# Kernel tuning notes

Measured on AMD Instinct MI355X. Metric: run time of the kernel, lower is better.

The kernel has to match this reference:

```python
import jax, jax.numpy as jnp
import numpy as np

K = 8            # hard-coded knn k
NS = 0.2         # LeakyReLU negative slope
EPS = 1e-6
LN_EPS = 1e-5
H = 6            # num_heads


def vn_lin(W, x):
    # VNLinear: linear over vector-channel dim (axis 1). x: (B, Cin, 3, ...)
    return jnp.einsum('oc,bc...->bo...', W, x)


def vn_leaky(x, W, U):
    # VNLinearLeakyReLU (no BN): feature map p, direction map d
    p = vn_lin(W, x)
    d = vn_lin(U, x)
    dot = jnp.sum(p * d, axis=2, keepdims=True)
    dsq = jnp.sum(d * d, axis=2, keepdims=True)
    neg = p - (dot / (dsq + EPS)) * d
    return NS * p + (1.0 - NS) * jnp.where(dot >= 0, p, neg)


def vn_layernorm(x, g, b):
    # LayerNorm on per-channel vector norms, rescale directions. x: (B,C,3,N)
    n = jnp.sqrt(jnp.sum(x * x, axis=2) + EPS)            # (B,C,N)
    mu = jnp.mean(n, axis=1, keepdims=True)
    var = jnp.var(n, axis=1, keepdims=True)
    nhat = (n - mu) / jnp.sqrt(var + LN_EPS)
    nnew = g[None, :, None] * nhat + b[None, :, None]
    return x * (nnew / n)[:, :, None, :]


def vn_attention(vn_x, Wq, Wk, Wv, Wo):
    # vn_x: (B, C, 3, N); VNLinear(C, 3C) projections, multi-head SDPA over N
    B, C, _, N = vn_x.shape
    def heads(W):
        t = vn_lin(W, vn_x)                               # (B, 3C, 3, N)
        t = t.reshape(B, H, 3 * C // H, 3, N)
        return t.transpose(0, 1, 4, 2, 3).reshape(B, H, N, -1)  # (B,H,N,9C/H)
    q, k, v = heads(Wq), heads(Wk), heads(Wv)
    scale = (3 * C // H) ** -0.5                          # head_dim = dim//H = 64
    attn = jax.nn.softmax(jnp.einsum('bhqd,bhkd->bhqk', q, k) * scale, axis=-1)
    o = jnp.einsum('bhqk,bhkd->bhqd', attn, v)            # (B,H,N,9C/H)
    o = o.transpose(0, 2, 1, 3).reshape(B, N, 3 * C, 3).transpose(0, 2, 3, 1)
    return vn_lin(Wo, o)                                  # (B, C, 3, N)


def vn_get_graph_feature(x, knn_index):
    # x: (B, C, 3, N); knn_index: flat (B*K*N,) into (B*N) rows
    B, C, _, N = x.shape
    xp = x.transpose(0, 3, 1, 2).reshape(B * N, C * 3)
    feat = xp[knn_index].reshape(B, K, N, C, 3)
    xc = x.transpose(0, 3, 1, 2).reshape(B, 1, N, C, 3)
    f = jnp.concatenate([feat - xc, jnp.broadcast_to(xc, (B, K, N, C, 3))], axis=3)
    return f.transpose(0, 3, 4, 2, 1)                     # (B, 2C, 3, N, K)


def setup_inputs() -> dict:
    key = jax.random.key(0)
    ks = jax.random.split(key, 20)
    B, N, C = 4, 2048, 128
    def w(k, o, i):
        return jax.random.normal(k, (o, i), jnp.float32) * (i ** -0.5)
    return {
        'x': jax.random.normal(ks[0], (B, N, 3 * C), jnp.float32),
        'knn_index': jax.random.randint(ks[1], (B * K * N,), 0, B * N),
        'g1': jnp.ones((C,), jnp.float32), 'b1': jnp.zeros((C,), jnp.float32),
        'g2': jnp.ones((C,), jnp.float32), 'b2': jnp.zeros((C,), jnp.float32),
        'Wq': w(ks[2], 3 * C, C), 'Wk': w(ks[3], 3 * C, C), 'Wv': w(ks[4], 3 * C, C),
        'Wo': w(ks[5], C, 3 * C),
        'W1': w(ks[6], C, 2 * C), 'U1': w(ks[7], C, 2 * C),   # conv1: 256->128
        'W2': w(ks[8], C, 2 * C),                               # conv2: 256->128
        'W3': w(ks[9], 2 * C, C), 'U3': w(ks[10], 2 * C, C),   # conv3: 128->256
        'W4': w(ks[11], C, 2 * C), 'U4': w(ks[12], C, 2 * C),  # conv4: 256->128
    }


def reference(x, knn_index, g1, b1, g2, b2, Wq, Wk, Wv, Wo, W1, U1, W2, W3, U3, W4, U4):
    B, N, D = x.shape
    C = D // 3
    vn_x = x.transpose(0, 2, 1).reshape(B, C, 3, N)
    norm_x = vn_layernorm(vn_x, g1, b1)
    x_1 = vn_attention(norm_x, Wq, Wk, Wv, Wo)            # (B,C,3,N)
    knn_f = vn_get_graph_feature(norm_x, knn_index)       # (B,2C,3,N,K)
    knn_f = vn_leaky(knn_f, W1, U1)                       # (B,C,3,N,K)
    knn_f = jnp.mean(knn_f, axis=-1)                      # mean_pool over k
    x_1 = jnp.concatenate([x_1, knn_f], axis=1)           # (B,2C,3,N)
    x_1 = vn_lin(W2, x_1)                                 # (B,C,3,N)
    vn_x = vn_x + x_1
    nx2 = vn_layernorm(vn_x, g2, b2)
    h = vn_leaky(nx2, W3, U3)                             # (B,2C,3,N)
    h = vn_leaky(h, W4, U4)                               # (B,C,3,N)
    vn_x = vn_x + h
    return vn_x.reshape(B, D, N).transpose(0, 2, 1)       # (B,N,384)
```

## Files before the change

### kernel.cpp

```cpp
#include <hip/hip_runtime.h>
#include <math.h>

#define NFIX 2048
#define HH 6
#define KNN 8
#define NSLOPE 0.2f
#define EPSF 1e-6f
#define LNEPSF 1e-5f
#define QSCALE 0.18033688011112042f

typedef unsigned short ushort_t;
typedef unsigned int uint_t;
typedef __attribute__((ext_vector_type(8))) short bf16x8;
typedef __attribute__((ext_vector_type(4))) short bf16x4;
typedef __attribute__((ext_vector_type(8))) _Float16 f16x8;
typedef __attribute__((ext_vector_type(4))) _Float16 f16x4;
typedef __attribute__((ext_vector_type(16))) float f32x16;
typedef __attribute__((ext_vector_type(4))) float f32x4;

__device__ __forceinline__ ushort_t f2bf(float f) {
  union { float f; unsigned u; } v; v.f = f;
  unsigned r = v.u + 0x7fff + ((v.u >> 16) & 1);
  return (ushort_t)(r >> 16);
}
__device__ __forceinline__ float bf2f(ushort_t u) {
  union { uint_t u; float f; } v; v.u = ((uint_t)u) << 16; return v.f;
}
__device__ __forceinline__ uint_t pack2(float a, float b) {
  return (uint_t)f2bf(a) | ((uint_t)f2bf(b) << 16);
}
__device__ __forceinline__ uint_t packh2(float a, float b) {
  union { _Float16 h; ushort_t s; } ha, hb;
  ha.h = (_Float16)a; hb.h = (_Float16)b;
  return (uint_t)ha.s | ((uint_t)hb.s << 16);
}

__device__ __forceinline__ void vnleaky3(const float* p, const float* dv, float* out) {
  float dot = p[0]*dv[0] + p[1]*dv[1] + p[2]*dv[2];
  float dsq = dv[0]*dv[0] + dv[1]*dv[1] + dv[2]*dv[2] + EPSF;
  float f = dot / dsq;
#pragma unroll
  for (int d = 0; d < 3; ++d) {
    float neg = p[d] - f * dv[d];
    out[d] = NSLOPE * p[d] + (1.f - NSLOPE) * ((dot >= 0.f) ? p[d] : neg);
  }
}

__global__ void prep_weights(const float* __restrict__ Wq, const float* __restrict__ Wk,
                             const float* __restrict__ Wv, const float* __restrict__ Wo,
                             const float* __restrict__ W1, const float* __restrict__ U1,
                             const float* __restrict__ W2, const float* __restrict__ W3,
                             const float* __restrict__ U3, const float* __restrict__ W4,
                             const float* __restrict__ U4,
                             ushort_t* __restrict__ Wall, _Float16* __restrict__ Af16,
                             _Float16* __restrict__ W3h, _Float16* __restrict__ U3h,
                             _Float16* __restrict__ W4h, _Float16* __restrict__ U4h) {
  int idx = blockIdx.x * 256 + threadIdx.x;
  if (idx < 212992) {
    int m = idx >> 7, c = idx & 127;
    float val;
    if (m < 384)       val = Wq[m*128 + c] * QSCALE;
    else if (m < 768)  val = Wk[(m-384)*128 + c];
    else if (m < 1152) val = Wv[(m-768)*128 + c];
    else {
      int j = m - 1152;
      if (j < 128)      val = W1[j*256 + c];
      else if (j < 256) val = U1[(j-128)*256 + c];
      else if (j < 384) { int o = j-256; val = W1[o*256 + 128 + c] - W1[o*256 + c]; }
      else              { int o = j-384; val = U1[o*256 + 128 + c] - U1[o*256 + c]; }
    }
    Wall[idx] = f2bf(val); return;
  }
  idx -= 212992;
  if (idx < 49152) {
    int j = idx / 128, c = idx % 128;
    float s = 0.f;
    for (int cp = 0; cp < 128; ++cp) s += W2[c*256 + cp] * Wo[cp*384 + j];
    Af16[(size_t)c*512 + j] = (_Float16)s; return;
  }
  idx -= 49152;
  if (idx < 16384) {
    int c2 = idx / 128, c = idx % 128;
    Af16[(size_t)c*512 + 384 + c2] = (_Float16)W2[c*256 + 128 + c2]; return;
  }
  idx -= 16384;
  if (idx < 32768) { W3h[idx] = (_Float16)W3[idx]; return; }
  idx -= 32768;
  if (idx < 32768) { U3h[idx] = (_Float16)U3[idx]; return; }
  idx -= 32768;
  if (idx < 32768) { W4h[idx] = (_Float16)W4[idx]; return; }
  idx -= 32768;
  if (idx < 32768) { U4h[idx] = (_Float16)U4[idx]; return; }
}

__global__ __launch_bounds__(128) void ln1_kernel(const float* __restrict__ in,
                                                  ushort_t* __restrict__ xbp,
                                                  float* __restrict__ xdi,
                                                  const float* __restrict__ g,
                                                  const float* __restrict__ b) {
  int bn = blockIdx.x;
  int c = threadIdx.x;
  const float* row = in + (size_t)bn * 384;
  float x0 = row[c*3+0], x1 = row[c*3+1], x2 = row[c*3+2];
  float nv = sqrtf(x0*x0 + x1*x1 + x2*x2 + EPSF);
  float s1 = nv, s2 = nv*nv;
#pragma unroll
  for (int off = 32; off >= 1; off >>= 1) {
    s1 += __shfl_down(s1, off);
    s2 += __shfl_down(s2, off);
  }
  __shared__ float red[4];
  int lane = threadIdx.x & 63, w = threadIdx.x >> 6;
  if (lane == 0) { red[w*2] = s1; red[w*2+1] = s2; }
  __syncthreads();
  float tot1 = red[0] + red[2], tot2 = red[1] + red[3];
  float mu  = tot1 * (1.f/128.f);
  float var = tot2 * (1.f/128.f) - mu*mu;
  float rsig = rsqrtf(var + LNEPSF);
  float nnew = g[c] * ((nv - mu) * rsig) + b[c];
  float sc = nnew / nv;
  size_t rb = (size_t)bn * 384;
  xbp[rb + c]       = f2bf(x0*sc);
  xbp[rb + 128 + c] = f2bf(x1*sc);
  xbp[rb + 256 + c] = f2bf(x2*sc);
  xdi[rb + c]       = x0;
  xdi[rb + 128 + c] = x1;
  xdi[rb + 256 + c] = x2;
}

__global__ __launch_bounds__(128) void ln2_kernel(const float* __restrict__ in,
                                                  _Float16* __restrict__ out,
                                                  const float* __restrict__ g,
                                                  const float* __restrict__ b) {
  int bn = blockIdx.x;
  int c = threadIdx.x;
  size_t base = (size_t)bn * 384;
  float x0 = in[base + c], x1 = in[base + 128 + c], x2 = in[base + 256 + c];
  float nv = sqrtf(x0*x0 + x1*x1 + x2*x2 + EPSF);
  float s1 = nv, s2 = nv*nv;
#pragma unroll
  for (int off = 32; off >= 1; off >>= 1) {
    s1 += __shfl_down(s1, off);
    s2 += __shfl_down(s2, off);
  }
  __shared__ float red[4];
  int lane = threadIdx.x & 63, w = threadIdx.x >> 6;
  if (lane == 0) { red[w*2] = s1; red[w*2+1] = s2; }
  __syncthreads();
  float tot1 = red[0] + red[2], tot2 = red[1] + red[3];
  float mu  = tot1 * (1.f/128.f);
  float var = tot2 * (1.f/128.f) - mu*mu;
  float rsig = rsqrtf(var + LNEPSF);
  float nnew = g[c] * ((nv - mu) * rsig) + b[c];
  float sc = nnew / nv;
  out[base + c]       = (_Float16)(x0*sc);
  out[base + 128 + c] = (_Float16)(x1*sc);
  out[base + 256 + c] = (_Float16)(x2*sc);
}

#define XT_PITCH 132
#define WT_PITCH 132
#define TR_PITCH 36
__global__ __launch_bounds__(256, 2) void qkv_conv1_mfma(
    const ushort_t* __restrict__ xb, const ushort_t* __restrict__ Wall,
    ushort_t* __restrict__ q, ushort_t* __restrict__ k, ushort_t* __restrict__ v,
    _Float16* __restrict__ YZh, _Float16* __restrict__ NBh) {
  __shared__ ushort_t xs[128*XT_PITCH];
  __shared__ ushort_t wt[32*WT_PITCH];
  __shared__ float tr[4][32*TR_PITCH];
  int nb = blockIdx.x % 192;
  int mq = blockIdx.x / 192;
  int n0 = nb * 128;
  int t = threadIdx.x;
  int w = t >> 6, lane = t & 63, ql = lane & 31, hl = lane >> 5;
  for (int idx = t; idx < 2048; idx += 256) {
    int n = idx >> 4, c16 = idx & 15;
    bf16x8 gv = *(const bf16x8*)&xb[(size_t)(n0 + n)*128 + c16*8];
    ushort_t* dst = &xs[n*XT_PITCH + c16*8];
    *(bf16x4*)dst = __builtin_shufflevector(gv, gv, 0, 1, 2, 3);
    *(bf16x4*)(dst+4) = __builtin_shufflevector(gv, gv, 4, 5, 6, 7);
  }
  __syncthreads();
  bf16x8 xf[8];
  {
    const ushort_t* xr = &xs[(w*32 + ql)*XT_PITCH + hl*8];
#pragma unroll
    for (int cs = 0; cs < 8; ++cs) {
      bf16x4 lo = *(const bf16x4*)(xr + cs*16);
      bf16x4 hi = *(const bf16x4*)(xr + cs*16 + 4);
      xf[cs] = __builtin_shufflevector(lo, hi, 0, 1, 2, 3, 4, 5, 6, 7);
    }
  }
  int ng = n0 + w*32 + ql;
  int pt = ng / 3;
  int d  = ng - 3*pt;
  float* trw = tr[w];
  for (int mt = 0; mt < 13; ++mt) {
    int m0 = mq*416 + mt*32;
    __syncthreads();
    for (int idx = t; idx < 512; idx += 256) {
      int mm = idx >> 4, c16 = idx & 15;
      bf16x8 gv = *(const bf16x8*)&Wall[(size_t)(m0 + mm)*128 + c16*8];
      ushort_t* dst = &wt[mm*WT_PITCH + c16*8];
      *(bf16x4*)dst = __builtin_shufflevector(gv, gv, 0, 1, 2, 3);
      *(bf16x4*)(dst+4) = __builtin_shufflevector(gv, gv, 4, 5, 6, 7);
    }
    __syncthreads();
    f32x16 acc;
#pragma unroll
    for (int r = 0; r < 16; ++r) acc[r] = 0.f;
    const ushort_t* wr = &wt[ql*WT_PITCH + hl*8];
#pragma unroll
    for (int cs = 0; cs < 8; ++cs) {
      bf16x4 lo = *(const bf16x4*)(wr + cs*16);
      bf16x4 hi = *(const bf16x4*)(wr + cs*16 + 4);
      bf16x8 af = __builtin_shufflevector(lo, hi, 0, 1, 2, 3, 4, 5, 6, 7);
      acc = __builtin_amdgcn_mfma_f32_32x32x16_bf16(af, xf[cs], acc, 0, 0, 0);
    }
#pragma unroll
    for (int r = 0; r < 16; ++r) {
      int mrow = (r&3) + 8*(r>>2) + 4*hl;
      trw[ql*TR_PITCH + mrow] = acc[r];
    }
    asm volatile("s_waitcnt lgkmcnt(0)" ::: "memory");
    float4 c0 = *(float4*)&trw[ql*TR_PITCH + hl*16 + 0];
    float4 c1 = *(float4*)&trw[ql*TR_PITCH + hl*16 + 4];
    float4 c2 = *(float4*)&trw[ql*TR_PITCH + hl*16 + 8];
    float4 c3 = *(float4*)&trw[ql*TR_PITCH + hl*16 + 12];
    asm volatile("s_waitcnt lgkmcnt(0)" ::: "memory");
    int mg = m0 + hl*16;
    if (m0 < 1152) {
      uint4 s0, s1;
      s0.x = pack2(c0.x, c0.y); s0.y = pack2(c0.z, c0.w);
      s0.z = pack2(c1.x, c1.y); s0.w = pack2(c1.z, c1.w);
      s1.x = pack2(c2.x, c2.y); s1.y = pack2(c2.z, c2.w);
      s1.z = pack2(c3.x, c3.y); s1.w = pack2(c3.z, c3.w);
      ushort_t* dst;
      if (m0 < 384)       dst = q + (size_t)pt*1152 + d*384 + mg;
      else if (m0 < 768)  dst = k + (size_t)pt*1152 + d*384 + (mg - 384);
      else                dst = v + (size_t)pt*1152 + d*384 + (mg - 768);
      *(uint4*)dst = s0;
      *(uint4*)(dst + 8) = s1;
    } else {
      int mat = mg - 1152;
      int sub = mat >> 7, o = mat & 127;
      _Float16* basep = (sub < 2) ? YZh : NBh;
      _Float16* dst = basep + (size_t)pt*768 + d*256 + (sub & 1)*128 + o;
      uint4 s0, s1;
      s0.x = packh2(c0.x, c0.y); s0.y = packh2(c0.z, c0.w);
      s0.z = packh2(c1.x, c1.y); s0.w = packh2(c1.z, c1.w);
      s1.x = packh2(c2.x, c2.y); s1.y = packh2(c2.z, c2.w);
      s1.z = packh2(c3.x, c3.y); s1.w = packh2(c3.z, c3.w);
      *(uint4*)dst = s0;
      *(uint4*)(dst + 8) = s1;
    }
  }
}

__global__ __launch_bounds__(128) void conv1_post(const _Float16* __restrict__ YZh,
    const _Float16* __restrict__ NBh, const int* __restrict__ knn_index,
    _Float16* __restrict__ kmf16) {
  int bn = blockIdx.x;
  int b = bn / NFIX, n = bn % NFIX;
  int t = threadIdx.x;
  __shared__ int sidx[KNN];
  if (t < KNN) sidx[t] = knn_index[(b*KNN + t)*NFIX + n];
  __syncthreads();
  float yb[3], zb[3];
#pragma unroll
  for (int d = 0; d < 3; ++d) {
    yb[d] = (float)NBh[(size_t)bn*768 + d*256 + t];
    zb[d] = (float)NBh[(size_t)bn*768 + d*256 + 128 + t];
  }
  float om[3] = {0.f, 0.f, 0.f};
#pragma unroll
  for (int kk = 0; kk < KNN; ++kk) {
    const _Float16* r = YZh + (size_t)sidx[kk]*768;
    float p[3], dd[3];
#pragma unroll
    for (int d = 0; d < 3; ++d) {
      p[d]  = (float)r[d*256 + t] + yb[d];
      dd[d] = (float)r[d*256 + 128 + t] + zb[d];
    }
    float res[3];
    vnleaky3(p, dd, res);
    om[0] += res[0]; om[1] += res[1]; om[2] += res[2];
  }
#pragma unroll
  for (int d = 0; d < 3; ++d)
    kmf16[((size_t)bn*3 + d)*128 + t] = (_Float16)(om[d] * (1.f/KNN));
}

#define VT_LP 196
__global__ __launch_bounds__(256) void vtrans_kernel(const ushort_t* __restrict__ v,
                                                     ushort_t* __restrict__ vT) {
  __shared__ ushort_t tl[64*VT_LP];
  int blk = blockIdx.x;
  int bh = blk / 32, ptile = blk % 32;
  int b = bh / HH, h = bh % HH;
  int pt0 = ptile * 64;
  int t = threadIdx.x;
#pragma unroll
  for (int i = 0; i < 6; ++i) {
    int u = i*256 + t;
    int p = u / 24, seg = u % 24;
    int d = seg >> 3, c8 = seg & 7;
    bf16x8 gv = *(const bf16x8*)&v[(size_t)(b*NFIX + pt0 + p)*1152 + d*384 + h*64 + c8*8];
    ushort_t* dst = &tl[p*VT_LP + d*64 + c8*8];
    *(bf16x4*)dst = __builtin_shufflevector(gv, gv, 0, 1, 2, 3);
    *(bf16x4*)(dst+4) = __builtin_shufflevector(gv, gv, 4, 5, 6, 7);
  }
  __syncthreads();
#pragma unroll
  for (int i = 0; i < 6; ++i) {
    int u = i*256 + t;
    int ch = u >> 3, pc = u & 7;
    int ol = ch / 3, dd = ch - 3*ol;
    int cloc = dd*64 + ol;
    ushort_t hv[8];
#pragma unroll
    for (int e = 0; e < 8; ++e)
      hv[e] = tl[(pc*8 + e)*VT_LP + cloc];
    uint4 o4;
    o4.x = (uint_t)hv[0] | ((uint_t)hv[1] << 16);
    o4.y = (uint_t)hv[2] | ((uint_t)hv[3] << 16);
    o4.z = (uint_t)hv[4] | ((uint_t)hv[5] << 16);
    o4.w = (uint_t)hv[6] | ((uint_t)hv[7] << 16);
    *(uint4*)&vT[((size_t)bh*192 + ch)*2048 + pt0 + pc*8] = o4;
  }
}

#define KT_P 196
#define VT_P 36
#define TW_P 195
__global__ __launch_bounds__(256, 2) void attn_kernel(const ushort_t* __restrict__ q,
    const ushort_t* __restrict__ k, const ushort_t* __restrict__ vT,
    ushort_t* __restrict__ opart, float* __restrict__ lpart) {
  __shared__ ushort_t kt[2][32*KT_P];
  __shared__ ushort_t vt[2][192*VT_P];
  __shared__ float alds[4][32];
  int blk = blockIdx.x;
  int qt = blk % 16;
  int bh = (blk / 16) % 24;
  int split = blk / (16*24);
  int b = bh / HH, h = bh % HH;
  int t = threadIdx.x;
  int w = t >> 6, lane = t & 63, ql = lane & 31, hl = lane >> 5;
  int qrow0 = qt*128 + w*32;
  const ushort_t* qpb = q + (size_t)(b*NFIX + qrow0 + ql)*1152 + h*64;
  bf16x8 qf[12];
#pragma unroll
  for (int cs = 0; cs < 12; ++cs) {
    int red0 = cs*16 + hl*8;
    int dq = red0 >> 6, ml = red0 & 63;
    qf[cs] = *(const bf16x8*)(qpb + dq*384 + ml);
  }
  const ushort_t* ksrc[3]; int kdsto[3];
  const ushort_t* vsrc[3]; int vdsto[3];
#pragma unroll
  for (int j = 0; j < 3; ++j) {
    int idx = t + j*256;
    int kp = idx / 24, c16 = idx % 24;
    int red0 = c16*8;
    int dk = red0 >> 6, ml = red0 & 63;
    ksrc[j] = k + (size_t)(b*NFIX + kp)*1152 + dk*384 + h*64 + ml;
    kdsto[j] = kp*KT_P + c16*8;
    int ch = idx >> 2, c4 = idx & 3;
    vsrc[j] = vT + ((size_t)bh*192 + ch)*2048 + c4*8;
    vdsto[j] = ch*VT_P + c4*8;
  }
  f32x16 acc[6];
#pragma unroll
  for (int nt = 0; nt < 6; ++nt)
#pragma unroll
    for (int r = 0; r < 16; ++r) acc[nt][r] = 0.f;
  float lsum = 0.f;
  int koff0 = split * 1024;
  bf16x8 kpre[3], vpre[3];
#pragma unroll
  for (int j = 0; j < 3; ++j) {
    kpre[j] = *(const bf16x8*)(ksrc[j] + (size_t)koff0*1152);
    vpre[j] = *(const bf16x8*)(vsrc[j] + koff0);
  }
#pragma unroll
  for (int j = 0; j < 3; ++j) {
    ushort_t* kd = &kt[0][kdsto[j]];
    *(bf16x4*)kd = __builtin_shufflevector(kpre[j], kpre[j], 0, 1, 2, 3);
    *(bf16x4*)(kd+4) = __builtin_shufflevector(kpre[j], kpre[j], 4, 5, 6, 7);
    ushort_t* vd = &vt[0][vdsto[j]];
    *(bf16x4*)vd = __builtin_shufflevector(vpre[j], vpre[j], 0, 1, 2, 3);
    *(bf16x4*)(vd+4) = __builtin_shufflevector(vpre[j], vpre[j], 4, 5, 6, 7);
  }
  __syncthreads();
  for (int kb = 0; kb < 32; ++kb) {
    int cur = kb & 1;
    if (kb < 31) {
      int koff = koff0 + (kb+1)*32;
#pragma unroll
      for (int j = 0; j < 3; ++j) {
        kpre[j] = *(const bf16x8*)(ksrc[j] + (size_t)koff*1152);
        vpre[j] = *(const bf16x8*)(vsrc[j] + koff);
      }
    }
    f32x16 sc;
#pragma unroll
    for (int r = 0; r < 16; ++r) sc[r] = 0.f;
    const ushort_t* ktc = kt[cur];
#pragma unroll
    for (int cs = 0; cs < 12; ++cs) {
      const ushort_t* kr = &ktc[ql*KT_P + cs*16 + hl*8];
      bf16x4 alo = *(const bf16x4*)kr;
      bf16x4 ahi = *(const bf16x4*)(kr + 4);
      bf16x8 af = __builtin_shufflevector(alo, ahi, 0, 1, 2, 3, 4, 5, 6, 7);
      sc = __builtin_amdgcn_mfma_f32_32x32x16_bf16(af, qf[cs], sc, 0, 0, 0);
    }
    uint_t u[8], pex[8];
#pragma unroll
    for (int g2 = 0; g2 < 4; ++g2) {
      float p0 = __builtin_amdgcn_exp2f(sc[g2*4 + 0]);
      float p1 = __builtin_amdgcn_exp2f(sc[g2*4 + 1]);
      float p2 = __builtin_amdgcn_exp2f(sc[g2*4 + 2]);
      float p3 = __builtin_amdgcn_exp2f(sc[g2*4 + 3]);
      lsum += (p0 + p1) + (p2 + p3);
      u[2*g2]   = pack2(p0, p1);
      u[2*g2+1] = pack2(p2, p3);
    }
#pragma unroll
    for (int j = 0; j < 8; ++j) pex[j] = (uint_t)__shfl_xor((int)u[j], 32);
    const ushort_t* vtc = vt[cur];
#pragma unroll
    for (int s = 0; s < 2; ++s) {
      uint4 au;
      au.x = hl ? pex[4*s+2] : u[4*s+0];
      au.y = hl ? pex[4*s+3] : u[4*s+1];
      au.z = hl ? u[4*s+2]   : pex[4*s+0];
      au.w = hl ? u[4*s+3]   : pex[4*s+1];
      union { uint4 ui; bf16x8 bv; } cvt; cvt.ui = au;
      bf16x8 pa = cvt.bv;
#pragma unroll
      for (int nt = 0; nt < 6; ++nt) {
        const ushort_t* vr = &vtc[(nt*32 + ql)*VT_P + s*16 + hl*8];
        bf16x4 vlo = *(const bf16x4*)vr;
        bf16x4 vhi = *(const bf16x4*)(vr + 4);
        bf16x8 vf = __builtin_shufflevector(vlo, vhi, 0, 1, 2, 3, 4, 5, 6, 7);
        acc[nt] = __builtin_amdgcn_mfma_f32_32x32x16_bf16(pa, vf, acc[nt], 0, 0, 0);
      }
    }
    if (kb < 31) {
      int nxt = cur ^ 1;
#pragma unroll
      for (int j = 0; j < 3; ++j) {
        ushort_t* kd = &kt[nxt][kdsto[j]];
        *(bf16x4*)kd = __builtin_shufflevector(kpre[j], kpre[j], 0, 1, 2, 3);
        *(bf16x4*)(kd+4) = __builtin_shufflevector(kpre[j], kpre[j], 4, 5, 6, 7);
        ushort_t* vd = &vt[nxt][vdsto[j]];
        *(bf16x4*)vd = __builtin_shufflevector(vpre[j], vpre[j], 0, 1, 2, 3);
        *(bf16x4*)(vd+4) = __builtin_shufflevector(vpre[j], vpre[j], 4, 5, 6, 7);
      }
    }
    __syncthreads();
  }
  lsum += __shfl_xor(lsum, 32);
  if (lane < 32) {
    alds[w][ql] = 1.0f / lsum;
    lpart[(size_t)split*24*NFIX + (size_t)bh*NFIX + qrow0 + ql] = lsum;
  }
  asm volatile("s_waitcnt lgkmcnt(0)" ::: "memory");
  float lv[4][4];
#pragma unroll
  for (int g2 = 0; g2 < 4; ++g2) {
    f32x4 tv = *(const f32x4*)&alds[w][8*g2 + 4*hl];
#pragma unroll
    for (int rr = 0; rr < 4; ++rr) lv[g2][rr] = tv[rr];
  }
  ushort_t* tw = (w == 0) ? kt[0] : (w == 1) ? kt[1] : (w == 2) ? vt[0] : vt[1];
#pragma unroll
  for (int nt = 0; nt < 6; ++nt) {
    int ch = nt*32 + ql;
#pragma unroll
    for (int r = 0; r < 16; ++r) {
      int qrow = (r&3) + 8*(r>>2) + 4*hl;
      tw[qrow*TW_P + ch] = f2bf(acc[nt][r] * lv[r>>2][r&3]);
    }
  }
  asm volatile("s_waitcnt lgkmcnt(0)" ::: "memory");
  const size_t SS = (size_t)8192*1152;
  ushort_t* opb = opart + (size_t)split*SS;
  size_t nbase = (size_t)(b*NFIX + qrow0) * 3;
#pragma unroll
  for (int i = 0; i < 12; ++i) {
    int chunk = i*64 + lane;
    int nl = chunk >> 3, jc = chunk & 7;
    int qq = nl / 3, dd = nl - 3*qq;
    ushort_t hv[8];
#pragma unroll
    for (int e = 0; e < 8; ++e)
      hv[e] = tw[qq*TW_P + (jc*8 + e)*3 + dd];
    uint4 sv;
    sv.x = (uint_t)hv[0] | ((uint_t)hv[1] << 16);
    sv.y = (uint_t)hv[2] | ((uint_t)hv[3] << 16);
    sv.z = (uint_t)hv[4] | ((uint_t)hv[5] << 16);
    sv.w = (uint_t)hv[6] | ((uint_t)hv[7] << 16);
    *(uint4*)&opb[(nbase + nl)*384 + h*64 + jc*8] = sv;
  }
}

#define AP 68
__global__ __launch_bounds__(384) void x1mid_mfma(
    const float* __restrict__ xdi, const ushort_t* __restrict__ opart,
    const float* __restrict__ lpart, const _Float16* __restrict__ kmf16,
    const _Float16* __restrict__ Af16, float* __restrict__ xmid) {
  __shared__ __align__(16) char smem[33536];
  _Float16* As = (_Float16*)smem;
  _Float16* Bt = (_Float16*)(smem + 17408);
  float* wlsL  = (float*)(smem + 30464);
  float* trbase = (float*)smem;
  int blk = blockIdx.x;
  int n0 = blk * 96;
  int pt0 = blk * 32;
  int t = threadIdx.x;
  int w = t >> 6, lane = t & 63, ql = lane & 31, hl = lane >> 5;
  int nsub = w >> 1, mh = w & 1;
  if (t < 192) {
    int ptl = t / 6, h = t % 6;
    int ptg = pt0 + ptl;
    int b = ptg >> 11, n = ptg & 2047;
    size_t lidx = (size_t)(b*HH + h)*NFIX + n;
    float l0 = lpart[lidx];
    float l1 = lpart[(size_t)24*NFIX + lidx];
    float rd = 1.f / (l0 + l1);
    float* wp = &wlsL[(ptl*6 + h)*2];
    wp[0] = l0*rd; wp[1] = l1*rd;
  }
  f32x16 acc[2];
#pragma unroll
  for (int m2 = 0; m2 < 2; ++m2)
#pragma unroll
    for (int r = 0; r < 16; ++r) acc[m2][r] = 0.f;
  const size_t SS = (size_t)8192*1152;
  __syncthreads();
  for (int p = 0; p < 8; ++p) {
    for (int u = t; u < 1024; u += 384) {
      int m = u >> 3, kc = u & 7;
      f16x4 a0 = *(const f16x4*)&Af16[(size_t)m*512 + p*64 + kc*8];
      f16x4 a1 = *(const f16x4*)&Af16[(size_t)m*512 + p*64 + kc*8 + 4];
      _Float16* dst = &As[m*AP + kc*8];
      *(f16x4*)dst = a0;
      *(f16x4*)(dst+4) = a1;
    }
    {
      int u = t;
      if (u < 384) {
        int n_l = u >> 2, jc = u & 3;
        int n_g = n0 + n_l;
        _Float16* dst = &Bt[n_l*AP + jc*16];
        if (p < 6) {
          int pt_l = n_l / 3;
          const float* wp = &wlsL[(pt_l*6 + p)*2];
          float facc[16];
#pragma unroll
          for (int e = 0; e < 16; ++e) facc[e] = 0.f;
#pragma unroll
          for (int s = 0; s < 2; ++s) {
            const ushort_t* src = opart + s*SS + (size_t)n_g*384 + p*64 + jc*16;
            uint4 ra = *(const uint4*)src;
            uint4 rb = *(const uint4*)(src + 8);
            const ushort_t* ua = (const ushort_t*)&ra;
            const ushort_t* ub = (const ushort_t*)&rb;
            float wsc = wp[s];
#pragma unroll
            for (int e = 0; e < 8; ++e) {
              facc[e]     += wsc * bf2f(ua[e]);
              facc[8 + e] += wsc * bf2f(ub[e]);
            }
          }
          _Float16 hv[16];
#pragma unroll
          for (int e = 0; e < 16; ++e) hv[e] = (_Float16)facc[e];
#pragma unroll
          for (int g = 0; g < 4; ++g)
            *(f16x4*)(dst + g*4) = *(f16x4*)&hv[g*4];
        } else {
          const _Float16* src = kmf16 + (size_t)n_g*128 + (p-6)*64 + jc*16;
          f16x4 v0 = *(const f16x4*)src;
          f16x4 v1 = *(const f16x4*)(src + 4);
          f16x4 v2 = *(const f16x4*)(src + 8);
          f16x4 v3 = *(const f16x4*)(src + 12);
          *(f16x4*)dst = v0; *(f16x4*)(dst+4) = v1;
          *(f16x4*)(dst+8) = v2; *(f16x4*)(dst+12) = v3;
        }
      }
    }
    __syncthreads();
#pragma unroll
    for (int cs = 0; cs < 4; ++cs) {
      int kloc = cs*16 + hl*8;
      f16x4 b0 = *(const f16x4*)&Bt[(nsub*32 + ql)*AP + kloc];
      f16x4 b1 = *(const f16x4*)&Bt[(nsub*32 + ql)*AP + kloc + 4];
      f16x8 bf = __builtin_shufflevector(b0, b1, 0, 1, 2, 3, 4, 5, 6, 7);
#pragma unroll
      for (int m2 = 0; m2 < 2; ++m2) {
        int mrow = (mh*2 + m2)*32 + ql;
        f16x4 a0 = *(const f16x4*)&As[mrow*AP + kloc];
        f16x4 a1 = *(const f16x4*)&As[mrow*AP + kloc + 4];
        f16x8 af = __builtin_shufflevector(a0, a1, 0, 1, 2, 3, 4, 5, 6, 7);
        acc[m2] = __builtin_amdgcn_mfma_f32_32x32x16_f16(af, bf, acc[m2], 0, 0, 0);
      }
    }
    __syncthreads();
  }
  float* trw = trbase + w*32*34;
#pragma unroll
  for (int m2 = 0; m2 < 2; ++m2) {
#pragma unroll
    for (int r = 0; r < 16; ++r) {
      int mrow = (r&3) + 8*(r>>2) + 4*hl;
      trw[ql*34 + mrow] = acc[m2][r];
    }
    asm volatile("s_waitcnt lgkmcnt(0)" ::: "memory");
    float4 c0 = *(float4*)&trw[ql*34 + hl*16 + 0];
    float4 c1 = *(float4*)&trw[ql*34 + hl*16 + 4];
    float4 c2 = *(float4*)&trw[ql*34 + hl*16 + 8];
    float4 c3 = *(float4*)&trw[ql*34 + hl*16 + 12];
    asm volatile("s_waitcnt lgkmcnt(0)" ::: "memory");
    int n_g = n0 + nsub*32 + ql;
    int c0g = (mh*2 + m2)*32 + hl*16;
    const float* xd = xdi + (size_t)n_g*128 + c0g;
    float4 x0 = *(const float4*)xd;
    float4 x1 = *(const float4*)(xd + 4);
    float4 x2 = *(const float4*)(xd + 8);
    float4 x3 = *(const float4*)(xd + 12);
    c0.x += x0.x; c0.y += x0.y; c0.z += x0.z; c0.w += x0.w;
    c1.x += x1.x; c1.y += x1.y; c1.z += x1.z; c1.w += x1.w;
    c2.x += x2.x; c2.y += x2.y; c2.z += x2.z; c2.w += x2.w;
    c3.x += x3.x; c3.y += x3.y; c3.z += x3.z; c3.w += x3.w;
    float* dst = xmid + (size_t)n_g*128 + c0g;
    *(float4*)dst = c0;
    *(float4*)(dst + 4) = c1;
    *(float4*)(dst + 8) = c2;
    *(float4*)(dst + 12) = c3;
  }
}

#define X3P 132
#define TR3P 36
__global__ __launch_bounds__(256) void conv3_mfma(const _Float16* __restrict__ nxh,
    const _Float16* __restrict__ W3h, const _Float16* __restrict__ U3h,
    _Float16* __restrict__ h3) {
  __shared__ __align__(16) _Float16 Xs[3*32*X3P];
  __shared__ __align__(16) _Float16 tr3[4][96*TR3P];
  int blk = blockIdx.x;
  int pt0 = (blk >> 1) * 32;
  int oh = blk & 1;
  int t = threadIdx.x;
  int w = t >> 6, lane = t & 63, ql = lane & 31, hl = lane >> 5;
#pragma unroll
  for (int i = 0; i < 6; ++i) {
    int u = i*256 + t;
    int r = u >> 4, c8 = u & 15;
    f16x8 gv = *(const f16x8*)&nxh[(size_t)(pt0*3 + r)*128 + c8*8];
    int d = r % 3, p = r / 3;
    _Float16* dst = &Xs[(d*32 + p)*X3P + c8*8];
    *(f16x4*)dst = __builtin_shufflevector(gv, gv, 0, 1, 2, 3);
    *(f16x4*)(dst+4) = __builtin_shufflevector(gv, gv, 4, 5, 6, 7);
  }
  __syncthreads();
  int ot = oh*128 + w*32;
  const _Float16* Wp = W3h + (size_t)(ot + ql)*128 + hl*8;
  const _Float16* Up = U3h + (size_t)(ot + ql)*128 + hl*8;
  f32x16 accP[3], accD[3];
#pragma unroll
  for (int d = 0; d < 3; ++d)
#pragma unroll
    for (int r = 0; r < 16; ++r) { accP[d][r] = 0.f; accD[d][r] = 0.f; }
#pragma unroll
  for (int cs = 0; cs < 8; ++cs) {
    f16x8 wf = *(const f16x8*)(Wp + cs*16);
    f16x8 uf = *(const f16x8*)(Up + cs*16);
#pragma unroll
    for (int d = 0; d < 3; ++d) {
      const _Float16* xr = &Xs[(d*32 + ql)*X3P + cs*16 + hl*8];
      f16x4 lo = *(const f16x4*)xr;
      f16x4 hi = *(const f16x4*)(xr + 4);
      f16x8 xf = __builtin_shufflevector(lo, hi, 0, 1, 2, 3, 4, 5, 6, 7);
      accP[d] = __builtin_amdgcn_mfma_f32_32x32x16_f16(wf, xf, accP[d], 0, 0, 0);
      accD[d] = __builtin_amdgcn_mfma_f32_32x32x16_f16(uf, xf, accD[d], 0, 0, 0);
    }
  }
  _Float16* trw = tr3[w];
#pragma unroll
  for (int r = 0; r < 16; ++r) {
    int olr = (r&3) + 8*(r>>2) + 4*hl;
    float p3[3], d3[3], res[3];
#pragma unroll
    for (int d = 0; d < 3; ++d) { p3[d] = accP[d][r]; d3[d] = accD[d][r]; }
    vnleaky3(p3, d3, res);
#pragma unroll
    for (int d = 0; d < 3; ++d) trw[(ql*3 + d)*TR3P + olr] = (_Float16)res[d];
  }
  asm volatile("s_waitcnt lgkmcnt(0)" ::: "memory");
#pragma unroll
  for (int i = 0; i < 6; ++i) {
    int u = i*64 + lane;
    int row = u >> 2, c8 = u & 3;
    const _Float16* src = &trw[row*TR3P + c8*8];
    f16x4 lo = *(const f16x4*)src;
    f16x4 hi = *(const f16x4*)(src + 4);
    f16x8 ov = __builtin_shufflevector(lo, hi, 0, 1, 2, 3, 4, 5, 6, 7);
    *(f16x8*)&h3[(size_t)(pt0*3 + row)*256 + ot + c8*8] = ov;
  }
}

#define X4P 260
#define TF4P 388
__global__ __launch_bounds__(256) void conv4_mfma(const _Float16* __restrict__ h3,
    const _Float16* __restrict__ W4h, const _Float16* __restrict__ U4h,
    const float* __restrict__ xmid, float* __restrict__ out) {
  __shared__ __align__(16) _Float16 Xs[3*16*X4P];
  __shared__ __align__(16) float trF[16*TF4P];
  int pt0 = blockIdx.x * 16;
  int t = threadIdx.x;
  int w = t >> 6, lane = t & 63;
  int nl = lane & 15, kq = lane >> 4;
#pragma unroll
  for (int i = 0; i < 6; ++i) {
    int u = i*256 + t;
    int r = u >> 5, c8 = u & 31;
    f16x8 gv = *(const f16x8*)&h3[(size_t)(pt0*3 + r)*256 + c8*8];
    int d = r % 3, p = r / 3;
    _Float16* dst = &Xs[(d*16 + p)*X4P + c8*8];
    *(f16x4*)dst = __builtin_shufflevector(gv, gv, 0, 1, 2, 3);
    *(f16x4*)(dst+4) = __builtin_shufflevector(gv, gv, 4, 5, 6, 7);
  }
  __syncthreads();
  int ot = w*32;
  f32x4 accP[2][3], accD[2][3];
#pragma unroll
  for (int mt = 0; mt < 2; ++mt)
#pragma unroll
    for (int d = 0; d < 3; ++d)
#pragma unroll
      for (int r = 0; r < 4; ++r) { accP[mt][d][r] = 0.f; accD[mt][d][r] = 0.f; }
  const _Float16* Wb = W4h + (size_t)ot*256;
  const _Float16* Ub = U4h + (size_t)ot*256;
#pragma unroll
  for (int cs = 0; cs < 8; ++cs) {
    int kof = cs*32 + kq*8;
    f16x8 xf[3];
#pragma unroll
    for (int d = 0; d < 3; ++d) {
      const _Float16* xr = &Xs[(d*16 + nl)*X4P + kof];
      f16x4 lo = *(const f16x4*)xr;
      f16x4 hi = *(const f16x4*)(xr + 4);
      xf[d] = __builtin_shufflevector(lo, hi, 0, 1, 2, 3, 4, 5, 6, 7);
    }
#pragma unroll
    for (int mt = 0; mt < 2; ++mt) {
      f16x8 wf = *(const f16x8*)(Wb + (size_t)(mt*16 + nl)*256 + kof);
      f16x8 uf = *(const f16x8*)(Ub + (size_t)(mt*16 + nl)*256 + kof);
#pragma unroll
      for (int d = 0; d < 3; ++d) {
        accP[mt][d] = __builtin_amdgcn_mfma_f32_16x16x32_f16(wf, xf[d], accP[mt][d], 0, 0, 0);
        accD[mt][d] = __builtin_amdgcn_mfma_f32_16x16x32_f16(uf, xf[d], accD[mt][d], 0, 0, 0);
      }
    }
  }
#pragma unroll
  for (int mt = 0; mt < 2; ++mt)
#pragma unroll
    for (int r = 0; r < 4; ++r) {
      int o = ot + mt*16 + kq*4 + r;
      float p3[3], d3[3], res[3];
#pragma unroll
      for (int d = 0; d < 3; ++d) { p3[d] = accP[mt][d][r]; d3[d] = accD[mt][d][r]; }
      vnleaky3(p3, d3, res);
#pragma unroll
      for (int d = 0; d < 3; ++d) trF[nl*TF4P + o*3 + d] = res[d];
    }
  __syncthreads();
#pragma unroll
  for (int i = 0; i < 6; ++i) {
    int u = i*256 + t;
    int row = u / 96, c4 = u % 96;
    float4 vv = *(float4*)&trF[row*TF4P + c4*4];
    int bn = pt0 + row;
    float rs[4];
    const float* fv = (const float*)&vv;
#pragma unroll
    for (int e = 0; e < 4; ++e) {
      int col = c4*4 + e;
      int o = col / 3, d = col - 3*o;
      rs[e] = fv[e] + xmid[(size_t)(3*bn + d)*128 + o];
    }
    float4 ov; ov.x = rs[0]; ov.y = rs[1]; ov.z = rs[2]; ov.w = rs[3];
    *(float4*)&out[(size_t)bn*384 + c4*4] = ov;
  }
}

extern "C" void kernel_launch(void* const* d_in, const int* in_sizes, int n_in,
                              void* d_out, int out_size, void* d_ws, size_t ws_size,
                              hipStream_t stream) {
  const float* x   = (const float*)d_in[0];
  const int* knn   = (const int*)d_in[1];
  const float* g1  = (const float*)d_in[2];
  const float* b1  = (const float*)d_in[3];
  const float* g2  = (const float*)d_in[4];
  const float* b2  = (const float*)d_in[5];
  const float* Wq  = (const float*)d_in[6];
  const float* Wk  = (const float*)d_in[7];
  const float* Wv  = (const float*)d_in[8];
  const float* Wo  = (const float*)d_in[9];
  const float* W1  = (const float*)d_in[10];
  const float* U1  = (const float*)d_in[11];
  const float* W2  = (const float*)d_in[12];
  const float* W3  = (const float*)d_in[13];
  const float* U3  = (const float*)d_in[14];
  const float* W4  = (const float*)d_in[15];
  const float* U4  = (const float*)d_in[16];
  float* out = (float*)d_out;
  (void)n_in; (void)out_size; (void)ws_size;

  const size_t BN = (size_t)in_sizes[0] / 384;

  float* ws    = (float*)d_ws;
  float* xdi   = ws;
  float* xmid  = xdi + BN*384;
  _Float16* kmf16 = (_Float16*)(xmid + BN*384);
  ushort_t* xbp = (ushort_t*)(kmf16 + BN*384);
  ushort_t* qb = xbp + BN*384;
  ushort_t* kb = qb + BN*1152;
  ushort_t* vb = kb + BN*1152;
  ushort_t* vT = vb + BN*1152;
  ushort_t* Wall = vT + BN*1152;
  _Float16* Af16 = (_Float16*)(Wall + 212992);
  _Float16* W3h = Af16 + 65536;
  _Float16* U3h = W3h + 32768;
  _Float16* W4h = U3h + 32768;
  _Float16* U4h = W4h + 32768;
  ushort_t* opart = (ushort_t*)(U4h + 32768);
  float* lpart = (float*)(opart + 4*BN*1152);
  _Float16* YZh = (_Float16*)opart;
  _Float16* NBh = YZh + BN*768;
  _Float16* nxh = (_Float16*)qb;
  _Float16* h3  = (_Float16*)kb;

  prep_weights<<<1600, 256, 0, stream>>>(Wq, Wk, Wv, Wo, W1, U1, W2, W3, U3, W4, U4,
                                         Wall, Af16, W3h, U3h, W4h, U4h);
  ln1_kernel<<<(int)BN, 128, 0, stream>>>(x, xbp, xdi, g1, b1);
  qkv_conv1_mfma<<<192*4, 256, 0, stream>>>(xbp, Wall, qb, kb, vb, YZh, NBh);
  conv1_post<<<(int)BN, 128, 0, stream>>>(YZh, NBh, knn, kmf16);
  vtrans_kernel<<<768, 256, 0, stream>>>(vb, vT);
  attn_kernel<<<16*24*2, 256, 0, stream>>>(qb, kb, vT, opart, lpart);
  x1mid_mfma<<<256, 384, 0, stream>>>(xdi, opart, lpart, kmf16, Af16, xmid);
  ln2_kernel<<<(int)BN, 128, 0, stream>>>(xmid, nxh, g2, b2);
  conv3_mfma<<<512, 256, 0, stream>>>(nxh, W3h, U3h, h3);
  conv4_mfma<<<512, 256, 0, stream>>>(h3, W4h, U4h, xmid, out);
}
```

Before: 336.9 us.

## Split attention over four key chunks with XCD-aware block mapping and dual accumulators

The attention key range is split into four chunks instead of two, which doubles the grid to 1536 blocks and halves the per-block loop length. The downstream x1mid kernel is generalised to merge NSPLIT partial outputs using their partial softmax sums. Block indices are remapped so that blocks sharing a batch-head sit on the same XCD, which should improve L2 reuse of K and V. The QK^T MFMA chain is split across two accumulators to shorten the dependency chain, and partial outputs are stored as fp16 instead of bf16 for better precision. The cost is more partial-output traffic and reduction work in x1mid, and the shared weight array there must be large enough for four splits.

```diff
diff --git a/kernel.cpp b/kernel.cpp
--- a/kernel.cpp
+++ b/kernel.cpp
@@ -8,6 +8,7 @@
 #define EPSF 1e-6f
 #define LNEPSF 1e-5f
 #define QSCALE 0.18033688011112042f
+#define NSPLIT 4
 
 typedef unsigned short ushort_t;
 typedef unsigned int uint_t;
@@ -28,6 +29,9 @@
 }
 __device__ __forceinline__ uint_t pack2(float a, float b) {
   return (uint_t)f2bf(a) | ((uint_t)f2bf(b) << 16);
+}
+__device__ __forceinline__ ushort_t f2h_bits(float a) {
+  union { _Float16 h; ushort_t s; } cv; cv.h = (_Float16)a; return cv.s;
 }
 __device__ __forceinline__ uint_t packh2(float a, float b) {
   union { _Float16 h; ushort_t s; } ha, hb;
@@ -340,9 +344,11 @@
   __shared__ ushort_t vt[2][192*VT_P];
   __shared__ float alds[4][32];
   int blk = blockIdx.x;
-  int qt = blk % 16;
-  int bh = (blk / 16) % 24;
-  int split = blk / (16*24);
+  int xcd = blk & 7, j = blk >> 3;
+  int g = xcd*12 + (j >> 4);
+  int qt = j & 15;
+  int bh = g % 24;
+  int split = g / 24;
   int b = bh / HH, h = bh % HH;
   int t = threadIdx.x;
   int w = t >> 6, lane = t & 63, ql = lane & 31, hl = lane >> 5;
@@ -358,16 +364,16 @@
   const ushort_t* ksrc[3]; int kdsto[3];
   const ushort_t* vsrc[3]; int vdsto[3];
 #pragma unroll
-  for (int j = 0; j < 3; ++j) {
-    int idx = t + j*256;
+  for (int j2 = 0; j2 < 3; ++j2) {
+    int idx = t + j2*256;
     int kp = idx / 24, c16 = idx % 24;
     int red0 = c16*8;
     int dk = red0 >> 6, ml = red0 & 63;
-    ksrc[j] = k + (size_t)(b*NFIX + kp)*1152 + dk*384 + h*64 + ml;
-    kdsto[j] = kp*KT_P + c16*8;
+    ksrc[j2] = k + (size_t)(b*NFIX + kp)*1152 + dk*384 + h*64 + ml;
+    kdsto[j2] = kp*KT_P + c16*8;
     int ch = idx >> 2, c4 = idx & 3;
-    vsrc[j] = vT + ((size_t)bh*192 + ch)*2048 + c4*8;
-    vdsto[j] = ch*VT_P + c4*8;
+    vsrc[j2] = vT + ((size_t)bh*192 + ch)*2048 + c4*8;
+    vdsto[j2] = ch*VT_P + c4*8;
   }
   f32x16 acc[6];
 #pragma unroll
@@ -375,36 +381,36 @@
 #pragma unroll
     for (int r = 0; r < 16; ++r) acc[nt][r] = 0.f;
   float lsum = 0.f;
-  int koff0 = split * 1024;
+  int koff0 = split * 512;
   bf16x8 kpre[3], vpre[3];
 #pragma unroll
-  for (int j = 0; j < 3; ++j) {
-    kpre[j] = *(const bf16x8*)(ksrc[j] + (size_t)koff0*1152);
-    vpre[j] = *(const bf16x8*)(vsrc[j] + koff0);
-  }
-#pragma unroll
-  for (int j = 0; j < 3; ++j) {
-    ushort_t* kd = &kt[0][kdsto[j]];
-    *(bf16x4*)kd = __builtin_shufflevector(kpre[j], kpre[j], 0, 1, 2, 3);
-    *(bf16x4*)(kd+4) = __builtin_shufflevector(kpre[j], kpre[j], 4, 5, 6, 7);
-    ushort_t* vd = &vt[0][vdsto[j]];
-    *(bf16x4*)vd = __builtin_shufflevector(vpre[j], vpre[j], 0, 1, 2, 3);
-    *(bf16x4*)(vd+4) = __builtin_shufflevector(vpre[j], vpre[j], 4, 5, 6, 7);
-  }
-  __syncthreads();
-  for (int kb = 0; kb < 32; ++kb) {
+  for (int j2 = 0; j2 < 3; ++j2) {
+    kpre[j2] = *(const bf16x8*)(ksrc[j2] + (size_t)koff0*1152);
+    vpre[j2] = *(const bf16x8*)(vsrc[j2] + koff0);
+  }
+#pragma unroll
+  for (int j2 = 0; j2 < 3; ++j2) {
+    ushort_t* kd = &kt[0][kdsto[j2]];
+    *(bf16x4*)kd = __builtin_shufflevector(kpre[j2], kpre[j2], 0, 1, 2, 3);
+    *(bf16x4*)(kd+4) = __builtin_shufflevector(kpre[j2], kpre[j2], 4, 5, 6, 7);
+    ushort_t* vd = &vt[0][vdsto[j2]];
+    *(bf16x4*)vd = __builtin_shufflevector(vpre[j2], vpre[j2], 0, 1, 2, 3);
+    *(bf16x4*)(vd+4) = __builtin_shufflevector(vpre[j2], vpre[j2], 4, 5, 6, 7);
+  }
+  __syncthreads();
+  for (int kb = 0; kb < 16; ++kb) {
     int cur = kb & 1;
-    if (kb < 31) {
+    if (kb < 15) {
       int koff = koff0 + (kb+1)*32;
 #pragma unroll
-      for (int j = 0; j < 3; ++j) {
-        kpre[j] = *(const bf16x8*)(ksrc[j] + (size_t)koff*1152);
-        vpre[j] = *(const bf16x8*)(vsrc[j] + koff);
+      for (int j2 = 0; j2 < 3; ++j2) {
+        kpre[j2] = *(const bf16x8*)(ksrc[j2] + (size_t)koff*1152);
+        vpre[j2] = *(const bf16x8*)(vsrc[j2] + koff);
       }
     }
-    f32x16 sc;
-#pragma unroll
-    for (int r = 0; r < 16; ++r) sc[r] = 0.f;
+    f32x16 sca, scb;
+#pragma unroll
+    for (int r = 0; r < 16; ++r) { sca[r] = 0.f; scb[r] = 0.f; }
     const ushort_t* ktc = kt[cur];
 #pragma unroll
     for (int cs = 0; cs < 12; ++cs) {
@@ -412,21 +418,22 @@
       bf16x4 alo = *(const bf16x4*)kr;
       bf16x4 ahi = *(const bf16x4*)(kr + 4);
       bf16x8 af = __builtin_shufflevector(alo, ahi, 0, 1, 2, 3, 4, 5, 6, 7);
-      sc = __builtin_amdgcn_mfma_f32_32x32x16_bf16(af, qf[cs], sc, 0, 0, 0);
+      if (cs & 1) scb = __builtin_amdgcn_mfma_f32_32x32x16_bf16(af, qf[cs], scb, 0, 0, 0);
+      else        sca = __builtin_amdgcn_mfma_f32_32x32x16_bf16(af, qf[cs], sca, 0, 0, 0);
     }
     uint_t u[8], pex[8];
 #pragma unroll
     for (int g2 = 0; g2 < 4; ++g2) {
-      float p0 = __builtin_amdgcn_exp2f(sc[g2*4 + 0]);
-      float p1 = __builtin_amdgcn_exp2f(sc[g2*4 + 1]);
-      float p2 = __builtin_amdgcn_exp2f(sc[g2*4 + 2]);
-      float p3 = __builtin_amdgcn_exp2f(sc[g2*4 + 3]);
+      float p0 = __builtin_amdgcn_exp2f(sca[g2*4 + 0] + scb[g2*4 + 0]);
+      float p1 = __builtin_amdgcn_exp2f(sca[g2*4 + 1] + scb[g2*4 + 1]);
+      float p2 = __builtin_amdgcn_exp2f(sca[g2*4 + 2] + scb[g2*4 + 2]);
+      float p3 = __builtin_amdgcn_exp2f(sca[g2*4 + 3] + scb[g2*4 + 3]);
       lsum += (p0 + p1) + (p2 + p3);
       u[2*g2]   = pack2(p0, p1);
       u[2*g2+1] = pack2(p2, p3);
     }
 #pragma unroll
-    for (int j = 0; j < 8; ++j) pex[j] = (uint_t)__shfl_xor((int)u[j], 32);
+    for (int j2 = 0; j2 < 8; ++j2) pex[j2] = (uint_t)__shfl_xor((int)u[j2], 32);
     const ushort_t* vtc = vt[cur];
 #pragma unroll
     for (int s = 0; s < 2; ++s) {
@@ -446,16 +453,16 @@
         acc[nt] = __builtin_amdgcn_mfma_f32_32x32x16_bf16(pa, vf, acc[nt], 0, 0, 0);
       }
     }
-    if (kb < 31) {
+    if (kb < 15) {
       int nxt = cur ^ 1;
 #pragma unroll
-      for (int j = 0; j < 3; ++j) {
-        ushort_t* kd = &kt[nxt][kdsto[j]];
-        *(bf16x4*)kd = __builtin_shufflevector(kpre[j], kpre[j], 0, 1, 2, 3);
-        *(bf16x4*)(kd+4) = __builtin_shufflevector(kpre[j], kpre[j], 4, 5, 6, 7);
-        ushort_t* vd = &vt[nxt][vdsto[j]];
-        *(bf16x4*)vd = __builtin_shufflevector(vpre[j], vpre[j], 0, 1, 2, 3);
-        *(bf16x4*)(vd+4) = __builtin_shufflevector(vpre[j], vpre[j], 4, 5, 6, 7);
+      for (int j2 = 0; j2 < 3; ++j2) {
+        ushort_t* kd = &kt[nxt][kdsto[j2]];
+        *(bf16x4*)kd = __builtin_shufflevector(kpre[j2], kpre[j2], 0, 1, 2, 3);
+        *(bf16x4*)(kd+4) = __builtin_shufflevector(kpre[j2], kpre[j2], 4, 5, 6, 7);
+        ushort_t* vd = &vt[nxt][vdsto[j2]];
+        *(bf16x4*)vd = __builtin_shufflevector(vpre[j2], vpre[j2], 0, 1, 2, 3);
+        *(bf16x4*)(vd+4) = __builtin_shufflevector(vpre[j2], vpre[j2], 4, 5, 6, 7);
       }
     }
     __syncthreads();
@@ -480,7 +487,7 @@
 #pragma unroll
     for (int r = 0; r < 16; ++r) {
       int qrow = (r&3) + 8*(r>>2) + 4*hl;
-      tw[qrow*TW_P + ch] = f2bf(acc[nt][r] * lv[r>>2][r&3]);
+      tw[qrow*TW_P + ch] = f2h_bits(acc[nt][r] * lv[r>>2][r&3]);
     }
   }
   asm volatile("s_waitcnt lgkmcnt(0)" ::: "memory");
@@ -526,11 +533,16 @@
     int ptg = pt0 + ptl;
     int b = ptg >> 11, n = ptg & 2047;
     size_t lidx = (size_t)(b*HH + h)*NFIX + n;
-    float l0 = lpart[lidx];
-    float l1 = lpart[(size_t)24*NFIX + lidx];
-    float rd = 1.f / (l0 + l1);
-    float* wp = &wlsL[(ptl*6 + h)*2];
-    wp[0] = l0*rd; wp[1] = l1*rd;
+    float l[NSPLIT]; float tot = 0.f;
+#pragma unroll
+    for (int s = 0; s < NSPLIT; ++s) {
+      l[s] = lpart[(size_t)s*24*NFIX + lidx];
+      tot += l[s];
+    }
+    float rd = 1.f / tot;
+    float* wp = &wlsL[(ptl*6 + h)*NSPLIT];
+#pragma unroll
+    for (int s = 0; s < NSPLIT; ++s) wp[s] = l[s]*rd;
   }
   f32x16 acc[2];
 #pragma unroll
@@ -556,22 +568,22 @@
         _Float16* dst = &Bt[n_l*AP + jc*16];
         if (p < 6) {
           int pt_l = n_l / 3;
-          const float* wp = &wlsL[(pt_l*6 + p)*2];
+          const float* wp = &wlsL[(pt_l*6 + p)*NSPLIT];
           float facc[16];
 #pragma unroll
           for (int e = 0; e < 16; ++e) facc[e] = 0.f;
 #pragma unroll
-          for (int s = 0; s < 2; ++s) {
+          for (int s = 0; s < NSPLIT; ++s) {
             const ushort_t* src = opart + s*SS + (size_t)n_g*384 + p*64 + jc*16;
             uint4 ra = *(const uint4*)src;
             uint4 rb = *(const uint4*)(src + 8);
-            const ushort_t* ua = (const ushort_t*)&ra;
-            const ushort_t* ub = (const ushort_t*)&rb;
+            const _Float16* ua = (const _Float16*)&ra;
+            const _Float16* ub = (const _Float16*)&rb;
             float wsc = wp[s];
 #pragma unroll
             for (int e = 0; e < 8; ++e) {
-              facc[e]     += wsc * bf2f(ua[e]);
-              facc[8 + e] += wsc * bf2f(ub[e]);
+              facc[e]     += wsc * (float)ua[e];
+              facc[8 + e] += wsc * (float)ub[e];
             }
           }
           _Float16 hv[16];
@@ -850,7 +862,7 @@
   qkv_conv1_mfma<<<192*4, 256, 0, stream>>>(xbp, Wall, qb, kb, vb, YZh, NBh);
   conv1_post<<<(int)BN, 128, 0, stream>>>(YZh, NBh, knn, kmf16);
   vtrans_kernel<<<768, 256, 0, stream>>>(vb, vT);
-  attn_kernel<<<16*24*2, 256, 0, stream>>>(qb, kb, vT, opart, lpart);
+  attn_kernel<<<16*24*NSPLIT, 256, 0, stream>>>(qb, kb, vT, opart, lpart);
   x1mid_mfma<<<256, 384, 0, stream>>>(xdi, opart, lpart, kmf16, Af16, xmid);
   ln2_kernel<<<(int)BN, 128, 0, stream>>>(xmid, nxh, g2, b2);
   conv3_mfma<<<512, 256, 0, stream>>>(nxh, W3h, U3h, h3);
```

New measurement: 337.5 us. No clear change (+0.2%).
